# Optimization experiments

Hardware: AMD Instinct MI355X
Metric: run time of the kernel (lower is better)

The kernel has to match this reference:

```python
import jax, jax.numpy as jnp
import numpy as np

N, B, D = 50000, 128, 35   # nodes, graphs, node_dim
T = 140                     # padded sequence length
EPS = 1e-5

def _gcn(x, W, b, src, dst):
    # PyG GCNConv: sym-normalized adjacency with self loops, then linear.
    h = x @ W
    deg = jnp.ones((N,), h.dtype).at[dst].add(1.0)  # in-degree + self loop
    dinv = jax.lax.rsqrt(deg)
    msg = h[src] * (dinv[src] * dinv[dst])[:, None]
    agg = jax.ops.segment_sum(msg, dst, num_segments=N)
    return agg + h * (dinv * dinv)[:, None] + b  # + self-loop messages + bias

def _bn(x, g, b):
    m = x.mean(0)
    v = x.var(0)
    return (x - m) * jax.lax.rsqrt(v + EPS) * g + b

def _lstm(xs, Wih, Whh, bih, bhh, reverse):
    # xs: [T, B, D]; torch LSTM gate order i,f,g,o; hidden size D
    def step(carry, xt):
        h, c = carry
        gates = xt @ Wih.T + h @ Whh.T + bih + bhh
        i, f, g, o = jnp.split(gates, 4, axis=-1)
        c = jax.nn.sigmoid(f) * c + jax.nn.sigmoid(i) * jnp.tanh(g)
        h = jax.nn.sigmoid(o) * jnp.tanh(c)
        return (h, c), h
    h0 = jnp.zeros((xs.shape[1], D), xs.dtype)
    _, hs = jax.lax.scan(step, (h0, h0), xs, reverse=reverse)
    return hs

def setup_inputs() -> dict:
    key = jax.random.key(0)
    ks = iter(jax.random.split(key, 64))
    def w(shape, s=0.05):
        return jax.random.normal(next(ks), shape, jnp.float32) * s
    inp = {
        'x': jax.random.normal(next(ks), (N, D), jnp.float32),
        'edge_intra': jax.random.randint(next(ks), (2, 300000), 0, N, jnp.int32),
        'edge_inter': jax.random.randint(next(ks), (2, 100000), 0, N, jnp.int32),
        'split': jax.random.randint(next(ks), (N,), 0, 2, jnp.int32),
        'batch': jnp.sort(jax.random.randint(next(ks), (N,), 0, B, jnp.int32)),
    }
    dims = [(35, 128), (128, 256), (256, 512), (512, 256), (256, 35)]
    for i, (di, do) in enumerate(dims, 1):
        inp[f'W{i}'] = w((di, do)); inp[f'b{i}'] = jnp.zeros((do,), jnp.float32)
        inp[f'g{i}'] = jnp.ones((do,), jnp.float32); inp[f'be{i}'] = jnp.zeros((do,), jnp.float32)
    for d in ('f', 'b'):  # bidirectional LSTM, 4*D = 140 gate rows
        inp[f'Wih_{d}'] = w((4 * D, D)); inp[f'Whh_{d}'] = w((4 * D, D))
        inp[f'bih_{d}'] = jnp.zeros((4 * D,), jnp.float32); inp[f'bhh_{d}'] = jnp.zeros((4 * D,), jnp.float32)
    for nm in ('q', 'k', 'v'):  # attention over d=2*D=70
        inp[f'W{nm}'] = w((2 * D, 2 * D)); inp[f'b{nm}'] = jnp.zeros((2 * D,), jnp.float32)
    inp['Wfc1'] = w((9800, 4340), 0.01); inp['bfc1'] = jnp.zeros((4340,), jnp.float32)
    inp['Wfc2'] = w((4340, 1), 0.01); inp['bfc2'] = jnp.zeros((1,), jnp.float32)
    return inp

def reference(x, edge_intra, edge_inter, split, batch,
              W1, b1, g1, be1, W2, b2, g2, be2, W3, b3, g3, be3,
              W4, b4, g4, be4, W5, b5, g5, be5,
              Wih_f, Whh_f, bih_f, bhh_f, Wih_b, Whh_b, bih_b, bhh_b,
              Wq, bq, Wk, bk, Wv, bv, Wfc1, bfc1, Wfc2, bfc2):
    src = jnp.concatenate([edge_intra[0], edge_inter[0]])
    dst = jnp.concatenate([edge_intra[1], edge_inter[1]])
    # conv1-3: relu then bn; conv4: bn then relu; conv5: bn only
    h = _bn(jax.nn.relu(_gcn(x, W1, b1, src, dst)), g1, be1)
    h = _bn(jax.nn.relu(_gcn(h, W2, b2, src, dst)), g2, be2)
    h = _bn(jax.nn.relu(_gcn(h, W3, b3, src, dst)), g3, be3)
    h = jax.nn.relu(_bn(_gcn(h, W4, b4, src, dst), g4, be4))
    h = _bn(_gcn(h, W5, b5, src, dst), g5, be5)
    # masked global_add_pool per split (avoids dynamic boolean indexing)
    is_pro = (split == 1).astype(h.dtype)[:, None]
    pro = jax.ops.segment_sum(h * is_pro, batch, num_segments=B)
    lig = jax.ops.segment_sum(h * (1.0 - is_pro), batch, num_segments=B)
    seq = jnp.concatenate([lig, pro], axis=1).reshape(B, 2, D)  # L = 2
    seq = jnp.pad(seq, ((0, 0), (0, T - 2), (0, 0)))            # [B,140,35]
    # attention mask, L=2 (static)
    m = jnp.eye(T, dtype=jnp.float32)
    m = m.at[2:, :].set(0.0).at[:, 2:].set(0.0)
    m = m.at[:, 1].set(1.0).at[1, :].set(1.0).at[1, 1].set(0.0)
    # BiLSTM over time axis
    xs = seq.transpose(1, 0, 2)  # [T,B,35]
    hf = _lstm(xs, Wih_f, Whh_f, bih_f, bhh_f, False)
    hb = _lstm(xs, Wih_b, Whh_b, bih_b, bhh_b, True)
    out = jnp.concatenate([hf, hb], axis=-1).transpose(1, 0, 2)  # [B,140,70]
    # masked single-head attention
    q = out @ Wq + bq
    k = out @ Wk + bk
    v = out @ Wv + bv
    sc = jnp.einsum('bqd,bkd->bqk', q, k) / jnp.sqrt(jnp.asarray(2.0 * D, out.dtype))
    sc = jnp.where(m[None] == 0, -1e9, sc)
    o = jax.nn.softmax(sc, axis=-1) @ v  # [B,140,70]
    f = jax.nn.relu(o.reshape(B, -1) @ Wfc1 + bfc1)
    return (f @ Wfc2 + bfc2).reshape(-1)
```

## Files before the change

kernel.cpp:

```cpp
#include <hip/hip_runtime.h>

#define N_NODES 50000
#define DIM0 35
#define BGRAPH 128
#define TSEQ 140
#define EPSBN 1e-5f
#define E_TOTAL 400000
#define E_INTRA 300000
#define E_INTER 100000
#define FC1_OUT 4340

typedef __attribute__((ext_vector_type(8))) short s8v;
typedef __attribute__((ext_vector_type(4))) short s4v;
typedef __attribute__((ext_vector_type(4))) float f32x4;

static __device__ __forceinline__ unsigned short bf16_rne(float x) {
    unsigned int u = __float_as_uint(x);
    unsigned int r = (u + 0x7FFFu + ((u >> 16) & 1u)) >> 16;
    return (unsigned short)r;
}
static __device__ __forceinline__ void bf16_split(float x, unsigned short& h, unsigned short& l) {
    h = bf16_rne(x);
    float hf = __uint_as_float(((unsigned int)h) << 16);
    l = bf16_rne(x - hf);
}

static __device__ __forceinline__ void edge_sd(int e, const int* intra, const int* inter, int& s, int& d) {
    if (e < E_INTRA) { s = intra[e]; d = intra[E_INTRA + e]; }
    else { int k = e - E_INTRA; s = inter[k]; d = inter[E_INTER + k]; }
}

__global__ void k_init(int* cnt, int* cursor, float* out, const float* bfc2, float* bnsumAll, float* bv4) {
    int i = blockIdx.x * 256 + threadIdx.x;
    if (i < N_NODES) { cnt[i] = 0; cursor[i] = 0; }
    if (i < BGRAPH) out[i] = bfc2[0];
    if (i < 5 * 1024) bnsumAll[i] = 0.f;
    if (i < 256) bv4[i] = 0.f;
}

__global__ void k_deg(const int* intra, const int* inter, int* cnt) {
    int e = blockIdx.x * 256 + threadIdx.x;
    if (e >= E_TOTAL) return;
    int s, d; edge_sd(e, intra, inter, s, d);
    atomicAdd(&cnt[d], 1);
}

__global__ void k_scan1(const int* __restrict__ cnt, int* __restrict__ partial, int* __restrict__ blocksum,
                        float* __restrict__ dinv) {
    __shared__ int buf[256];
    int t = threadIdx.x;
    int i = blockIdx.x * 256 + t;
    int v = (i < N_NODES) ? cnt[i] : 0;
    if (i < N_NODES) dinv[i] = rsqrtf(1.0f + (float)v);
    buf[t] = v;
    __syncthreads();
    for (int off = 1; off < 256; off <<= 1) {
        int add = (t >= off) ? buf[t - off] : 0;
        __syncthreads();
        buf[t] += add;
        __syncthreads();
    }
    if (i < N_NODES) partial[i] = buf[t];
    if (t == 255) blocksum[blockIdx.x] = buf[255];
}

__global__ void k_scan2(int* blocksum, int nb) {
    __shared__ int buf[256];
    int t = threadIdx.x;
    buf[t] = (t < nb) ? blocksum[t] : 0;
    __syncthreads();
    for (int off = 1; off < 256; off <<= 1) {
        int add = (t >= off) ? buf[t - off] : 0;
        __syncthreads();
        buf[t] += add;
        __syncthreads();
    }
    if (t < nb) blocksum[t] = buf[t];
}

__global__ void k_scan3(const int* __restrict__ partial, const int* __restrict__ blocksum, int* __restrict__ rowptr) {
    int b = blockIdx.x;
    int i = b * 256 + threadIdx.x;
    if (i == 0) rowptr[0] = 0;
    if (i < N_NODES) {
        int off = (b == 0) ? 0 : blocksum[b - 1];
        rowptr[i + 1] = partial[i] + off;
    }
}

__global__ void k_scatter(const int* intra, const int* inter, const int* rowptr,
                          int* cursor, const float* dinv, int* srcs, float* coef) {
    int e = blockIdx.x * 256 + threadIdx.x;
    if (e >= E_TOTAL) return;
    int s, d; edge_sd(e, intra, inter, s, d);
    int p = rowptr[d] + atomicAdd(&cursor[d], 1);
    srcs[p] = s;
    coef[p] = dinv[s] * dinv[d];
}

__global__ __launch_bounds__(256) void k_agg_small(const float* __restrict__ X, float* __restrict__ Z,
        const int* __restrict__ rowptr, const int* __restrict__ srcs, const float* __restrict__ coef,
        const float* __restrict__ dinv, const float* __restrict__ bias) {
    int wave = threadIdx.x >> 6, lane = threadIdx.x & 63;
    int i = blockIdx.x * 4 + wave;
    if (i >= N_NODES || lane >= DIM0) return;
    int b0 = rowptr[i], e1 = rowptr[i + 1];
    float self = dinv[i] * dinv[i];
    float acc = X[(size_t)i * DIM0 + lane] * self;
    if (bias) acc += bias[lane];
    for (int k = b0; k < e1; ++k) acc += coef[k] * X[(size_t)srcs[k] * DIM0 + lane];
    Z[(size_t)i * DIM0 + lane] = acc;
}

__global__ __launch_bounds__(256) void k_agg_vec(const float* __restrict__ X, float* __restrict__ Z,
        const int* __restrict__ rowptr, const int* __restrict__ srcs, const float* __restrict__ coef,
        const float* __restrict__ dinv, const float* __restrict__ alpha, const float* __restrict__ beta,
        const float* __restrict__ bias, int d, int lpshift) {
    int i = (blockIdx.x * 256 + threadIdx.x) >> lpshift;
    int lane_in = threadIdx.x & ((1 << lpshift) - 1);
    if (i >= N_NODES) return;
    int b0 = rowptr[i], e1 = rowptr[i + 1];
    float self = dinv[i] * dinv[i];
    int c = lane_in * 4;
    float4 al, be;
    if (alpha) { al = *(const float4*)&alpha[c]; be = *(const float4*)&beta[c]; }
    else { al = make_float4(1.f, 1.f, 1.f, 1.f); be = make_float4(0.f, 0.f, 0.f, 0.f); }
    float4 xi = *(const float4*)&X[(size_t)i * d + c];
    float4 acc;
    acc.x = self * (al.x * xi.x + be.x);
    acc.y = self * (al.y * xi.y + be.y);
    acc.z = self * (al.z * xi.z + be.z);
    acc.w = self * (al.w * xi.w + be.w);
    if (bias) {
        float4 bi = *(const float4*)&bias[c];
        acc.x += bi.x; acc.y += bi.y; acc.z += bi.z; acc.w += bi.w;
    }
    for (int k = b0; k < e1; ++k) {
        int s = srcs[k];
        float cf = coef[k];
        float4 xs = *(const float4*)&X[(size_t)s * d + c];
        acc.x += cf * (al.x * xs.x + be.x);
        acc.y += cf * (al.y * xs.y + be.y);
        acc.z += cf * (al.z * xs.z + be.z);
        acc.w += cf * (al.w * xs.w + be.w);
    }
    *(float4*)&Z[(size_t)i * d + c] = acc;
}

__global__ __launch_bounds__(256) void k_gemm(const float* __restrict__ A, const float* __restrict__ W,
                                              const float* __restrict__ bias, float* __restrict__ C,
                                              int Mrows, int K, int Ncols, int relu,
                                              const float* __restrict__ alphaA, const float* __restrict__ betaA,
                                              int reluA) {
    __shared__ float As[64][17];
    __shared__ float Ws[16][65];
    int tid = threadIdx.x;
    int tx = tid & 15, ty = tid >> 4;
    int row0 = blockIdx.y * 64, col0 = blockIdx.x * 64;
    float acc[4][4] = {};
    for (int k0 = 0; k0 < K; k0 += 16) {
        for (int l = tid; l < 1024; l += 256) {
            int m = l >> 4, kk = l & 15;
            int r = row0 + m, k = k0 + kk;
            float v = 0.f;
            if (r < Mrows && k < K) {
                v = A[(size_t)r * K + k];
                if (alphaA) {
                    v = alphaA[k] * v + betaA[k];
                    if (reluA) v = fmaxf(v, 0.f);
                }
            }
            As[m][kk] = v;
        }
        for (int l = tid; l < 1024; l += 256) {
            int kk = l >> 6, n = l & 63;
            int k = k0 + kk, c = col0 + n;
            Ws[kk][n] = (k < K && c < Ncols) ? W[(size_t)k * Ncols + c] : 0.f;
        }
        __syncthreads();
#pragma unroll
        for (int kk = 0; kk < 16; ++kk) {
            float a[4], w[4];
#pragma unroll
            for (int i2 = 0; i2 < 4; ++i2) a[i2] = As[ty * 4 + i2][kk];
#pragma unroll
            for (int j = 0; j < 4; ++j) w[j] = Ws[kk][tx * 4 + j];
#pragma unroll
            for (int i2 = 0; i2 < 4; ++i2)
#pragma unroll
                for (int j = 0; j < 4; ++j)
                    acc[i2][j] += a[i2] * w[j];
        }
        __syncthreads();
    }
    for (int i2 = 0; i2 < 4; ++i2) {
        int r = row0 + ty * 4 + i2;
        if (r >= Mrows) continue;
        for (int j = 0; j < 4; ++j) {
            int c = col0 + tx * 4 + j;
            if (c >= Ncols) continue;
            float v = acc[i2][j];
            if (bias) v += bias[c];
            if (relu) v = fmaxf(v, 0.f);
            C[(size_t)r * Ncols + c] = v;
        }
    }
}

__global__ void k_wprep(const float* __restrict__ W, unsigned short* __restrict__ Wf, int K, int Ncols,
                        const float* __restrict__ rowscale) {
    int gid = blockIdx.x * 256 + threadIdx.x;
    int KT = K >> 5;
    int total = (Ncols >> 4) * KT * 64;
    if (gid >= total) return;
    int lane = gid & 63;
    int f = gid >> 6;
    int kt = f % KT, ntile = f / KT;
    int n = ntile * 16 + (lane & 15);
    int kb = kt * 32 + (lane >> 4) * 8;
    size_t base = (size_t)f * 1024 + lane * 8;
#pragma unroll
    for (int j = 0; j < 8; ++j) {
        float v = W[(size_t)(kb + j) * Ncols + n];
        if (rowscale) v *= rowscale[kb + j];
        unsigned short h, l;
        bf16_split(v, h, l);
        Wf[base + j] = h;
        Wf[base + 512 + j] = l;
    }
}

__global__ void k_bnbias(const float* __restrict__ W, const float* __restrict__ beta,
                         float* __restrict__ bv, int K, int Ncols) {
    int c = threadIdx.x;
    if (c >= Ncols) return;
    int k0 = blockIdx.x * 16;
    float acc = 0.f;
#pragma unroll
    for (int k = 0; k < 16; ++k) acc += beta[k0 + k] * W[(size_t)(k0 + k) * Ncols + c];
    atomicAdd(&bv[c], acc);
}

__global__ __launch_bounds__(256) void k_gemm_mfma(
    const float* __restrict__ A, const unsigned short* __restrict__ Wf,
    const float* __restrict__ bias, float* __restrict__ C,
    int Mrows, int K, int Ncols, int relu,
    const float* __restrict__ alphaA, const float* __restrict__ betaA,
    float* __restrict__ bnsum) {
    __shared__ unsigned short As[2][2][128][40];
    int tid = threadIdx.x;
    int lane = tid & 63, wave = tid >> 6;
    int wm = wave >> 1, wn = wave & 1;
    int row0 = blockIdx.y * 128;
    int nt0 = blockIdx.x * 8;
    int KT = K >> 5;

    f32x4 acc[4][4];
#pragma unroll
    for (int a = 0; a < 4; ++a)
#pragma unroll
        for (int b = 0; b < 4; ++b) acc[a][b] = (f32x4)0.f;

    float4 reg[4];
    auto load_chunk = [&](int kt) {
#pragma unroll
        for (int l = 0; l < 4; ++l) {
            int i = tid + l * 256;
            int m = i >> 3, kv = (i & 7) * 4;
            int r = row0 + m;
            float4 v = make_float4(0.f, 0.f, 0.f, 0.f);
            if (r < Mrows) v = *(const float4*)&A[(size_t)r * K + kt * 32 + kv];
            reg[l] = v;
        }
    };
    auto store_chunk = [&](int buf, int kt) {
#pragma unroll
        for (int l = 0; l < 4; ++l) {
            int i = tid + l * 256;
            int m = i >> 3, kv = (i & 7) * 4;
            float4 v = reg[l];
            if (alphaA) {
                int kg = kt * 32 + kv;
                float4 al = *(const float4*)&alphaA[kg];
                float4 be = *(const float4*)&betaA[kg];
                v.x = al.x * v.x + be.x;
                v.y = al.y * v.y + be.y;
                v.z = al.z * v.z + be.z;
                v.w = al.w * v.w + be.w;
            }
            unsigned short h0, l0, h1, l1, h2, l2, h3, l3;
            bf16_split(v.x, h0, l0); bf16_split(v.y, h1, l1);
            bf16_split(v.z, h2, l2); bf16_split(v.w, h3, l3);
            s4v hv = {(short)h0, (short)h1, (short)h2, (short)h3};
            s4v lv = {(short)l0, (short)l1, (short)l2, (short)l3};
            *(s4v*)&As[buf][0][m][kv] = hv;
            *(s4v*)&As[buf][1][m][kv] = lv;
        }
    };
    auto loadW = [&](int kt, s8v (&bh)[4], s8v (&bl)[4]) {
#pragma unroll
        for (int nt = 0; nt < 4; ++nt) {
            int ntg = nt0 + wn * 4 + nt;
            size_t fb = ((size_t)(ntg * KT + kt)) * 1024 + lane * 8;
            bh[nt] = *(const s8v*)&Wf[fb];
            bl[nt] = *(const s8v*)&Wf[fb + 512];
        }
    };

    int mrow = wm * 64 + (lane & 15);
    int koff = (lane >> 4) * 8;

    s8v bhA[4], blA[4], bhB[4], blB[4];
    load_chunk(0);
    store_chunk(0, 0);
    loadW(0, bhA, blA);
    __syncthreads();

    auto phase = [&](int kt, int cur, s8v (&bh)[4], s8v (&bl)[4], s8v (&nbh)[4], s8v (&nbl)[4]) {
        if (kt + 1 < KT) {
            load_chunk(kt + 1);
            loadW(kt + 1, nbh, nbl);
        }
        s8v ah[4], alo[4];
#pragma unroll
        for (int mt = 0; mt < 4; ++mt) {
            ah[mt]  = *(const s8v*)&As[cur][0][mrow + mt * 16][koff];
            alo[mt] = *(const s8v*)&As[cur][1][mrow + mt * 16][koff];
        }
#pragma unroll
        for (int nt = 0; nt < 4; ++nt)
#pragma unroll
            for (int mt = 0; mt < 4; ++mt) {
                acc[mt][nt] = __builtin_amdgcn_mfma_f32_16x16x32_bf16(ah[mt], bh[nt], acc[mt][nt], 0, 0, 0);
                acc[mt][nt] = __builtin_amdgcn_mfma_f32_16x16x32_bf16(ah[mt], bl[nt], acc[mt][nt], 0, 0, 0);
                acc[mt][nt] = __builtin_amdgcn_mfma_f32_16x16x32_bf16(alo[mt], bh[nt], acc[mt][nt], 0, 0, 0);
            }
        if (kt + 1 < KT) store_chunk(cur ^ 1, kt + 1);
        __syncthreads();
    };

    for (int kt = 0; kt < KT; kt += 2) {
        phase(kt, 0, bhA, blA, bhB, blB);
        phase(kt + 1, 1, bhB, blB, bhA, blA);
    }

    int cbase = (nt0 + wn * 4) * 16 + (lane & 15);
    float bia[4];
#pragma unroll
    for (int nt = 0; nt < 4; ++nt) bia[nt] = bias ? bias[cbase + nt * 16] : 0.f;
    float s1[4] = {0.f, 0.f, 0.f, 0.f}, s2[4] = {0.f, 0.f, 0.f, 0.f};
#pragma unroll
    for (int mt = 0; mt < 4; ++mt) {
        int rbase = row0 + wm * 64 + mt * 16 + (lane >> 4) * 4;
#pragma unroll
        for (int r = 0; r < 4; ++r) {
            int rg = rbase + r;
            if (rg < Mrows) {
#pragma unroll
                for (int nt = 0; nt < 4; ++nt) {
                    float v = acc[mt][nt][r] + bia[nt];
                    if (relu) v = fmaxf(v, 0.f);
                    C[(size_t)rg * Ncols + cbase + nt * 16] = v;
                    s1[nt] += v; s2[nt] += v * v;
                }
            }
        }
    }
    if (bnsum) {
#pragma unroll
        for (int nt = 0; nt < 4; ++nt) {
            float a = s1[nt], b = s2[nt];
            a += __shfl_xor(a, 16, 64);
            a += __shfl_xor(a, 32, 64);
            b += __shfl_xor(b, 16, 64);
            b += __shfl_xor(b, 32, 64);
            if (lane < 16) {
                atomicAdd(&bnsum[cbase + nt * 16], a);
                atomicAdd(&bnsum[Ncols + cbase + nt * 16], b);
            }
        }
    }
}

__global__ void k_bn_stats(const float* __restrict__ X, float* sums, int d) {
    long long total = (long long)N_NODES * d;
    int G = gridDim.x * blockDim.x;
    int gid = blockIdx.x * blockDim.x + threadIdx.x;
    int c = gid % d;
    float s1 = 0.f, s2 = 0.f;
    for (long long i = gid; i < total; i += G) {
        float v = X[i];
        s1 += v; s2 += v * v;
    }
    atomicAdd(&sums[c], s1);
    atomicAdd(&sums[d + c], s2);
}

__global__ void k_bn_final(const float* sums, const float* g, const float* be,
                           float* alpha, float* beta, int d) {
    int c = threadIdx.x;
    if (c >= d) return;
    float mean = sums[c] / (float)N_NODES;
    float var = sums[d + c] / (float)N_NODES - mean * mean;
    float a = g[c] * rsqrtf(var + EPSBN);
    alpha[c] = a;
    beta[c] = be[c] - mean * a;
}

__global__ void k_pool(const float* __restrict__ h, const int* __restrict__ split,
                       const int* __restrict__ batch, float* lig, float* pro,
                       const float* __restrict__ alpha, const float* __restrict__ beta) {
    int b = blockIdx.x;
    __shared__ float sl[DIM0], sp[DIM0];
    __shared__ int s_start, s_end;
    if (threadIdx.x < DIM0) { sl[threadIdx.x] = 0.f; sp[threadIdx.x] = 0.f; }
    if (threadIdx.x == 0) {
        int lo = 0, hi = N_NODES;
        while (lo < hi) { int mid = (lo + hi) >> 1; if (batch[mid] < b) lo = mid + 1; else hi = mid; }
        s_start = lo;
        hi = N_NODES;
        while (lo < hi) { int mid = (lo + hi) >> 1; if (batch[mid] < b + 1) lo = mid + 1; else hi = mid; }
        s_end = lo;
    }
    __syncthreads();
    int start = s_start, end = s_end;
    for (int k = threadIdx.x; k < (end - start) * DIM0; k += blockDim.x) {
        int node = start + k / DIM0;
        int c = k % DIM0;
        float v = alpha[c] * h[(size_t)node * DIM0 + c] + beta[c];
        if (split[node] == 1) atomicAdd(&sp[c], v);
        else atomicAdd(&sl[c], v);
    }
    __syncthreads();
    if (threadIdx.x < DIM0) {
        lig[b * DIM0 + threadIdx.x] = sl[threadIdx.x];
        pro[b * DIM0 + threadIdx.x] = sp[threadIdx.x];
    }
}

__global__ __launch_bounds__(192) void k_lstm(
    const float* __restrict__ lig, const float* __restrict__ pro,
    const float* __restrict__ Wih_f, const float* __restrict__ Whh_f,
    const float* __restrict__ bih_f, const float* __restrict__ bhh_f,
    const float* __restrict__ Wih_b, const float* __restrict__ Whh_b,
    const float* __restrict__ bih_b, const float* __restrict__ bhh_b,
    float* __restrict__ outb) {
    int blk = blockIdx.x;
    int dir = blk >> 7;
    int b = blk & 127;
    const float* Wih = dir ? Wih_b : Wih_f;
    const float* Whh = dir ? Whh_b : Whh_f;
    const float* bih = dir ? bih_b : bih_f;
    const float* bhh = dir ? bhh_b : bhh_f;

    __shared__ float h_lds[DIM0];
    __shared__ float x_lds[2][DIM0];
    __shared__ float gate_lds[4 * DIM0];
    int t = threadIdx.x;
    float wih[DIM0], whh[DIM0], bsum = 0.f;
    if (t < 4 * DIM0) {
#pragma unroll
        for (int j = 0; j < DIM0; ++j) { wih[j] = Wih[t * DIM0 + j]; whh[j] = Whh[t * DIM0 + j]; }
        bsum = bih[t] + bhh[t];
    }
    if (t < DIM0) {
        x_lds[0][t] = lig[b * DIM0 + t];
        x_lds[1][t] = pro[b * DIM0 + t];
        h_lds[t] = 0.f;
    }
    float c_reg = 0.f;
    __syncthreads();
    for (int step = 0; step < TSEQ; ++step) {
        int tt = dir ? (TSEQ - 1 - step) : step;
        if (t < 4 * DIM0) {
            float acc = bsum;
            if (tt < 2) {
#pragma unroll
                for (int j = 0; j < DIM0; ++j) acc += wih[j] * x_lds[tt][j];
            }
#pragma unroll
            for (int j = 0; j < DIM0; ++j) acc += whh[j] * h_lds[j];
            gate_lds[t] = acc;
        }
        __syncthreads();
        if (t < DIM0) {
            float gi = gate_lds[t], gf = gate_lds[DIM0 + t];
            float gg = gate_lds[2 * DIM0 + t], go = gate_lds[3 * DIM0 + t];
            float si = 1.f / (1.f + expf(-gi));
            float sf = 1.f / (1.f + expf(-gf));
            float so = 1.f / (1.f + expf(-go));
            c_reg = sf * c_reg + si * tanhf(gg);
            float hv = so * tanhf(c_reg);
            h_lds[t] = hv;
            outb[((size_t)b * TSEQ + tt) * 70 + dir * DIM0 + t] = hv;
        }
        __syncthreads();
    }
}

__global__ void k_concatW(const float* __restrict__ Wq, const float* __restrict__ bq,
                          const float* __restrict__ Wk, const float* __restrict__ bk,
                          const float* __restrict__ Wv, const float* __restrict__ bv,
                          float* __restrict__ Wcat, float* __restrict__ bcat) {
    int idx = blockIdx.x * 256 + threadIdx.x;
    if (idx < 70 * 210) {
        int k = idx / 210, col = idx % 210;
        int g = col / 70, j = col % 70;
        const float* Wsrc = (g == 0) ? Wq : ((g == 1) ? Wk : Wv);
        Wcat[idx] = Wsrc[k * 70 + j];
    }
    if (idx < 210) {
        int g = idx / 70, j = idx % 70;
        const float* bsrc = (g == 0) ? bq : ((g == 1) ? bk : bv);
        bcat[idx] = bsrc[j];
    }
}

__global__ void k_attention(const float* __restrict__ qkv, float* __restrict__ osm) {
    int b = blockIdx.x;
    __shared__ float q0[70], q1[70], s[TSEQ];
    __shared__ float s00_s, s01_s, ssum_s;
    int t = threadIdx.x;
    const float* base = qkv + (size_t)b * TSEQ * 210;
    if (t < 70) {
        q0[t] = base[0 * 210 + t];
        q1[t] = base[1 * 210 + t];
    }
    __syncthreads();
    const float scale = rsqrtf(70.f);
    if (t < TSEQ) {
        const float* krow = base + (size_t)t * 210 + 70;
        float acc = 0.f;
        for (int j = 0; j < 70; ++j) acc += q1[j] * krow[j];
        s[t] = acc * scale;
    } else if (t == TSEQ || t == TSEQ + 1) {
        int kk = t - TSEQ;
        const float* krow = base + (size_t)kk * 210 + 70;
        float acc = 0.f;
        for (int j = 0; j < 70; ++j) acc += q0[j] * krow[j];
        if (kk) s01_s = acc * scale; else s00_s = acc * scale;
    }
    __syncthreads();
    if (t == 0) {
        float mx = -1e30f;
        for (int i = 0; i < TSEQ; ++i) if (i != 1) mx = fmaxf(mx, s[i]);
        float sum = 0.f;
        for (int i = 0; i < TSEQ; ++i) {
            float e = (i == 1) ? 0.f : expf(s[i] - mx);
            s[i] = e; sum += e;
        }
        ssum_s = sum;
    }
    __syncthreads();
    if (t < 70) {
        float inv = 1.f / ssum_s;
        float acc = 0.f;
        for (int i = 0; i < TSEQ; ++i) acc += s[i] * base[(size_t)i * 210 + 140 + t];
        float o1v = acc * inv;
        float m0 = fmaxf(s00_s, s01_s);
        float e0 = expf(s00_s - m0), e1 = expf(s01_s - m0);
        float w0 = e0 / (e0 + e1), w1 = e1 / (e0 + e1);
        float v0 = base[0 * 210 + 140 + t];
        float v1 = base[1 * 210 + 140 + t];
        osm[b * 210 + t] = w0 * v0 + w1 * v1;
        osm[b * 210 + 70 + t] = o1v;
        osm[b * 210 + 140 + t] = v1;
    }
}

__global__ void k_wsum(const float* __restrict__ Wfc1, float* __restrict__ Wsum) {
    int idx = blockIdx.x * 256 + threadIdx.x;
    if (idx >= 70 * FC1_OUT) return;
    int j = idx / FC1_OUT, c = idx % FC1_OUT;
    float acc = 0.f;
    for (int tt = 2; tt < TSEQ; ++tt) acc += Wfc1[((size_t)(tt * 70 + j)) * FC1_OUT + c];
    Wsum[(size_t)j * FC1_OUT + c] = acc;
}

__global__ __launch_bounds__(256) void k_fc(const float* __restrict__ osm, const float* __restrict__ Wfc1,
                                            const float* __restrict__ Wsum, const float* __restrict__ bfc1,
                                            const float* __restrict__ Wfc2, float* __restrict__ out) {
    __shared__ float olds[8][210];
    __shared__ float wred[4][8];
    int g = blockIdx.y;
    int c = blockIdx.x * 256 + threadIdx.x;
    for (int l = threadIdx.x; l < 8 * 210; l += 256)
        olds[l / 210][l % 210] = osm[(g * 8 + l / 210) * 210 + (l % 210)];
    __syncthreads();
    float acc[8] = {};
    if (c < FC1_OUT) {
        for (int j = 0; j < 140; ++j) {
            float w = Wfc1[(size_t)j * FC1_OUT + c];
#pragma unroll
            for (int b = 0; b < 8; ++b) acc[b] = fmaf(olds[b][j], w, acc[b]);
        }
        for (int j = 0; j < 70; ++j) {
            float w = Wsum[(size_t)j * FC1_OUT + c];
#pragma unroll
            for (int b = 0; b < 8; ++b) acc[b] = fmaf(olds[b][140 + j], w, acc[b]);
        }
        float bb = bfc1[c], pw = Wfc2[c];
#pragma unroll
        for (int b = 0; b < 8; ++b) acc[b] = fmaxf(acc[b] + bb, 0.f) * pw;
    }
#pragma unroll
    for (int b = 0; b < 8; ++b) {
        acc[b] += __shfl_down(acc[b], 32, 64);
        acc[b] += __shfl_down(acc[b], 16, 64);
        acc[b] += __shfl_down(acc[b], 8, 64);
        acc[b] += __shfl_down(acc[b], 4, 64);
        acc[b] += __shfl_down(acc[b], 2, 64);
        acc[b] += __shfl_down(acc[b], 1, 64);
    }
    int wave = threadIdx.x >> 6;
    if ((threadIdx.x & 63) == 0)
#pragma unroll
        for (int b = 0; b < 8; ++b) wred[wave][b] = acc[b];
    __syncthreads();
    if (threadIdx.x < 8) {
        float t = wred[0][threadIdx.x] + wred[1][threadIdx.x] + wred[2][threadIdx.x] + wred[3][threadIdx.x];
        atomicAdd(&out[g * 8 + threadIdx.x], t);
    }
}

extern "C" void kernel_launch(void* const* d_in, const int* in_sizes, int n_in,
                              void* d_out, int out_size, void* d_ws, size_t ws_size,
                              hipStream_t stream) {
    const float* x = (const float*)d_in[0];
    const int* intra = (const int*)d_in[1];
    const int* inter = (const int*)d_in[2];
    const int* split = (const int*)d_in[3];
    const int* batch = (const int*)d_in[4];
    const float *W[5], *bW[5], *gW[5], *beW[5];
    for (int i = 0; i < 5; ++i) {
        W[i]   = (const float*)d_in[5 + 4 * i];
        bW[i]  = (const float*)d_in[6 + 4 * i];
        gW[i]  = (const float*)d_in[7 + 4 * i];
        beW[i] = (const float*)d_in[8 + 4 * i];
    }
    const float* Wih_f = (const float*)d_in[25];
    const float* Whh_f = (const float*)d_in[26];
    const float* bih_f = (const float*)d_in[27];
    const float* bhh_f = (const float*)d_in[28];
    const float* Wih_b = (const float*)d_in[29];
    const float* Whh_b = (const float*)d_in[30];
    const float* bih_b = (const float*)d_in[31];
    const float* bhh_b = (const float*)d_in[32];
    const float* Wq = (const float*)d_in[33];
    const float* bq = (const float*)d_in[34];
    const float* Wk = (const float*)d_in[35];
    const float* bk = (const float*)d_in[36];
    const float* Wv = (const float*)d_in[37];
    const float* bv = (const float*)d_in[38];
    const float* Wfc1 = (const float*)d_in[39];
    const float* bfc1 = (const float*)d_in[40];
    const float* Wfc2 = (const float*)d_in[41];
    const float* bfc2 = (const float*)d_in[42];

    char* p = (char*)d_ws;
    auto carve = [&](size_t bytes) {
        char* r = p;
        p += (bytes + 255) & ~(size_t)255;
        return r;
    };
    float* bufA = (float*)carve((size_t)N_NODES * 512 * 4);
    float* bufB = (float*)carve((size_t)N_NODES * 256 * 4);
    float* bufM = (float*)carve((size_t)N_NODES * 256 * 4);
    float* dinv = (float*)carve((size_t)N_NODES * 4);
    int* cnt    = (int*)carve((size_t)N_NODES * 4);
    int* rowptr = (int*)carve((size_t)(N_NODES + 1) * 4);
    int* cursor = (int*)carve((size_t)N_NODES * 4);
    int* scanp  = (int*)carve((size_t)N_NODES * 4);
    int* bsums  = (int*)carve(256 * 4);
    int* srcs   = (int*)carve((size_t)E_TOTAL * 4);
    float* coef = (float*)carve((size_t)E_TOTAL * 4);
    float* bnsumAll = (float*)carve(5 * 1024 * 4);
    float* alphaAll = (float*)carve(5 * 512 * 4);
    float* betaAll  = (float*)carve(5 * 512 * 4);
    float* bv4  = (float*)carve(256 * 4);
    float* lig = (float*)carve((size_t)BGRAPH * DIM0 * 4);
    float* pro = (float*)carve((size_t)BGRAPH * DIM0 * 4);
    float* outb = (float*)carve((size_t)BGRAPH * TSEQ * 70 * 4);
    float* qkvb = (float*)carve((size_t)BGRAPH * TSEQ * 210 * 4);
    float* Wcat = (float*)carve((size_t)70 * 210 * 4);
    float* bcat = (float*)carve(210 * 4);
    float* osm = (float*)carve((size_t)BGRAPH * 210 * 4);
    float* wsum = (float*)carve((size_t)70 * FC1_OUT * 4);
    unsigned short* Wf2 = (unsigned short*)carve((size_t)128 * 256 * 2 * 2);
    unsigned short* Wf3 = (unsigned short*)carve((size_t)256 * 512 * 2 * 2);
    unsigned short* Wf4 = (unsigned short*)carve((size_t)512 * 256 * 2 * 2);

    float* out = (float*)d_out;

    const int SCAN_B = (N_NODES + 255) / 256;

    k_init<<<(N_NODES + 255) / 256, 256, 0, stream>>>(cnt, cursor, out, bfc2, bnsumAll, bv4);
    k_deg<<<(E_TOTAL + 255) / 256, 256, 0, stream>>>(intra, inter, cnt);
    k_scan1<<<SCAN_B, 256, 0, stream>>>(cnt, scanp, bsums, dinv);
    k_scan2<<<1, 256, 0, stream>>>(bsums, SCAN_B);
    k_scan3<<<SCAN_B, 256, 0, stream>>>(scanp, bsums, rowptr);
    k_scatter<<<(E_TOTAL + 255) / 256, 256, 0, stream>>>(intra, inter, rowptr, cursor, dinv, srcs, coef);
    k_concatW<<<(70 * 210 + 255) / 256, 256, 0, stream>>>(Wq, bq, Wk, bk, Wv, bv, Wcat, bcat);
    k_wprep<<<((256 / 16) * (128 / 32) * 64 + 255) / 256, 256, 0, stream>>>(W[1], Wf2, 128, 256, nullptr);
    k_wprep<<<((512 / 16) * (256 / 32) * 64 + 255) / 256, 256, 0, stream>>>(W[2], Wf3, 256, 512, nullptr);

    auto BN = [&](int layer) { return bnsumAll + layer * 1024; };
    auto AL = [&](int layer) { return alphaAll + layer * 512; };
    auto BE = [&](int layer) { return betaAll + layer * 512; };
    auto bn_final = [&](int layer, int d) {
        k_bn_final<<<1, 512, 0, stream>>>(BN(layer), gW[layer], beW[layer], AL(layer), BE(layer), d);
    };

    const int GB64 = (N_NODES + 63) / 64;
    const int GB128 = (N_NODES + 127) / 128;
    const int AGG4 = (N_NODES + 3) / 4;
    const int AGG8 = (N_NODES + 7) / 8;

    k_agg_small<<<AGG4, 256, 0, stream>>>(x, bufM, rowptr, srcs, coef, dinv, nullptr);
    k_gemm<<<dim3(2, GB64), 256, 0, stream>>>(bufM, W[0], bW[0], bufA, N_NODES, 35, 128, 1, nullptr, nullptr, 0);
    k_bn_stats<<<128, 256, 0, stream>>>(bufA, BN(0), 128);
    bn_final(0, 128);
    k_agg_vec<<<AGG8, 256, 0, stream>>>(bufA, bufM, rowptr, srcs, coef, dinv, AL(0), BE(0), nullptr, 128, 5);
    k_gemm_mfma<<<dim3(2, GB128), 256, 0, stream>>>(bufM, Wf2, bW[1], bufB, N_NODES, 128, 256, 1,
                                                    nullptr, nullptr, BN(1));
    bn_final(1, 256);
    k_agg_vec<<<AGG4, 256, 0, stream>>>(bufB, bufM, rowptr, srcs, coef, dinv, AL(1), BE(1), nullptr, 256, 6);
    k_gemm_mfma<<<dim3(4, GB128), 256, 0, stream>>>(bufM, Wf3, bW[2], bufA, N_NODES, 256, 512, 1,
                                                    nullptr, nullptr, BN(2));
    bn_final(2, 512);
    k_wprep<<<((256 / 16) * (512 / 32) * 64 + 255) / 256, 256, 0, stream>>>(W[3], Wf4, 512, 256, AL(2));
    k_bnbias<<<512 / 16, 256, 0, stream>>>(W[3], BE(2), bv4, 512, 256);
    k_gemm_mfma<<<dim3(2, GB128), 256, 0, stream>>>(bufA, Wf4, bv4, bufM, N_NODES, 512, 256, 0,
                                                    nullptr, nullptr, nullptr);
    k_agg_vec<<<AGG4, 256, 0, stream>>>(bufM, bufB, rowptr, srcs, coef, dinv, nullptr, nullptr, bW[3], 256, 6);
    k_bn_stats<<<256, 256, 0, stream>>>(bufB, BN(3), 256);
    bn_final(3, 256);
    k_gemm<<<dim3(1, GB64), 256, 0, stream>>>(bufB, W[4], nullptr, bufM, N_NODES, 256, 35, 0, AL(3), BE(3), 1);
    k_agg_small<<<AGG4, 256, 0, stream>>>(bufM, bufA, rowptr, srcs, coef, dinv, bW[4]);
    k_bn_stats<<<35, 256, 0, stream>>>(bufA, BN(4), 35);
    bn_final(4, 35);

    k_pool<<<BGRAPH, 256, 0, stream>>>(bufA, split, batch, lig, pro, AL(4), BE(4));

    k_lstm<<<256, 192, 0, stream>>>(lig, pro, Wih_f, Whh_f, bih_f, bhh_f,
                                    Wih_b, Whh_b, bih_b, bhh_b, outb);

    k_gemm<<<dim3(4, (BGRAPH * TSEQ + 63) / 64), 256, 0, stream>>>(outb, Wcat, bcat, qkvb,
                                                                   BGRAPH * TSEQ, 70, 210, 0, nullptr, nullptr, 0);

    k_attention<<<BGRAPH, 256, 0, stream>>>(qkvb, osm);

    k_wsum<<<(70 * FC1_OUT + 255) / 256, 256, 0, stream>>>(Wfc1, wsum);
    k_fc<<<dim3(17, 16), 256, 0, stream>>>(osm, Wfc1, wsum, bfc1, Wfc2, out);
}
```

Measured before the change: 1.017 ms.

## Fuse BN finalize into consumers, fold BN stats into GEMM, misc tweaks

Removes the separate k_bn_final launches and recomputes the BN scale/shift inline from the raw sums wherever they are consumed (aggregation, GEMM loaders, weight prep, pool). The first layer's k_bn_stats pass is folded into the scalar GEMM epilogue through shared-memory and global atomics. Edge-loop bounds in the aggregation kernels are made wave-uniform with readfirstlane, and the LSTM recurrent dot product is split across two accumulators to shorten the dependency chain. The cost is redundant per-element rsqrt work in hot loaders and extra atomics in the GEMM epilogue.

```diff
diff --git a/kernel.cpp b/kernel.cpp
--- a/kernel.cpp
+++ b/kernel.cpp
@@ -24,6 +24,14 @@
     float hf = __uint_as_float(((unsigned int)h) << 16);
     l = bf16_rne(x - hf);
 }
+static __device__ __forceinline__ void bn_ab(const float* __restrict__ bnsum, const float* __restrict__ g,
+                                             const float* __restrict__ be, int d, int c, float& a, float& b) {
+    const float invN = 1.0f / (float)N_NODES;
+    float mean = bnsum[c] * invN;
+    float var = bnsum[d + c] * invN - mean * mean;
+    a = g[c] * rsqrtf(var + EPSBN);
+    b = be[c] - mean * a;
+}
 
 static __device__ __forceinline__ void edge_sd(int e, const int* intra, const int* inter, int& s, int& d) {
     if (e < E_INTRA) { s = intra[e]; d = intra[E_INTRA + e]; }
@@ -104,7 +112,8 @@
     int wave = threadIdx.x >> 6, lane = threadIdx.x & 63;
     int i = blockIdx.x * 4 + wave;
     if (i >= N_NODES || lane >= DIM0) return;
-    int b0 = rowptr[i], e1 = rowptr[i + 1];
+    int b0 = __builtin_amdgcn_readfirstlane(rowptr[i]);
+    int e1 = __builtin_amdgcn_readfirstlane(rowptr[i + 1]);
     float self = dinv[i] * dinv[i];
     float acc = X[(size_t)i * DIM0 + lane] * self;
     if (bias) acc += bias[lane];
@@ -114,23 +123,32 @@
 
 __global__ __launch_bounds__(256) void k_agg_vec(const float* __restrict__ X, float* __restrict__ Z,
         const int* __restrict__ rowptr, const int* __restrict__ srcs, const float* __restrict__ coef,
-        const float* __restrict__ dinv, const float* __restrict__ alpha, const float* __restrict__ beta,
-        const float* __restrict__ bias, int d, int lpshift) {
+        const float* __restrict__ dinv, const float* __restrict__ bnsum, const float* __restrict__ g,
+        const float* __restrict__ be, const float* __restrict__ bias, int d, int lpshift) {
     int i = (blockIdx.x * 256 + threadIdx.x) >> lpshift;
     int lane_in = threadIdx.x & ((1 << lpshift) - 1);
     if (i >= N_NODES) return;
     int b0 = rowptr[i], e1 = rowptr[i + 1];
+    if (lpshift == 6) {
+        b0 = __builtin_amdgcn_readfirstlane(b0);
+        e1 = __builtin_amdgcn_readfirstlane(e1);
+    }
     float self = dinv[i] * dinv[i];
     int c = lane_in * 4;
-    float4 al, be;
-    if (alpha) { al = *(const float4*)&alpha[c]; be = *(const float4*)&beta[c]; }
-    else { al = make_float4(1.f, 1.f, 1.f, 1.f); be = make_float4(0.f, 0.f, 0.f, 0.f); }
+    float4 al = make_float4(1.f, 1.f, 1.f, 1.f);
+    float4 bb = make_float4(0.f, 0.f, 0.f, 0.f);
+    if (bnsum) {
+        bn_ab(bnsum, g, be, d, c + 0, al.x, bb.x);
+        bn_ab(bnsum, g, be, d, c + 1, al.y, bb.y);
+        bn_ab(bnsum, g, be, d, c + 2, al.z, bb.z);
+        bn_ab(bnsum, g, be, d, c + 3, al.w, bb.w);
+    }
     float4 xi = *(const float4*)&X[(size_t)i * d + c];
     float4 acc;
-    acc.x = self * (al.x * xi.x + be.x);
-    acc.y = self * (al.y * xi.y + be.y);
-    acc.z = self * (al.z * xi.z + be.z);
-    acc.w = self * (al.w * xi.w + be.w);
+    acc.x = self * (al.x * xi.x + bb.x);
+    acc.y = self * (al.y * xi.y + bb.y);
+    acc.z = self * (al.z * xi.z + bb.z);
+    acc.w = self * (al.w * xi.w + bb.w);
     if (bias) {
         float4 bi = *(const float4*)&bias[c];
         acc.x += bi.x; acc.y += bi.y; acc.z += bi.z; acc.w += bi.w;
@@ -139,10 +157,10 @@
         int s = srcs[k];
         float cf = coef[k];
         float4 xs = *(const float4*)&X[(size_t)s * d + c];
-        acc.x += cf * (al.x * xs.x + be.x);
-        acc.y += cf * (al.y * xs.y + be.y);
-        acc.z += cf * (al.z * xs.z + be.z);
-        acc.w += cf * (al.w * xs.w + be.w);
+        acc.x += cf * (al.x * xs.x + bb.x);
+        acc.y += cf * (al.y * xs.y + bb.y);
+        acc.z += cf * (al.z * xs.z + bb.z);
+        acc.w += cf * (al.w * xs.w + bb.w);
     }
     *(float4*)&Z[(size_t)i * d + c] = acc;
 }
@@ -150,13 +168,16 @@
 __global__ __launch_bounds__(256) void k_gemm(const float* __restrict__ A, const float* __restrict__ W,
                                               const float* __restrict__ bias, float* __restrict__ C,
                                               int Mrows, int K, int Ncols, int relu,
-                                              const float* __restrict__ alphaA, const float* __restrict__ betaA,
-                                              int reluA) {
+                                              const float* __restrict__ bnA, const float* __restrict__ gA,
+                                              const float* __restrict__ beA, int reluA,
+                                              float* __restrict__ bnsumOut) {
     __shared__ float As[64][17];
     __shared__ float Ws[16][65];
+    __shared__ float sl_s[64], sq_s[64];
     int tid = threadIdx.x;
     int tx = tid & 15, ty = tid >> 4;
     int row0 = blockIdx.y * 64, col0 = blockIdx.x * 64;
+    if (tid < 64) { sl_s[tid] = 0.f; sq_s[tid] = 0.f; }
     float acc[4][4] = {};
     for (int k0 = 0; k0 < K; k0 += 16) {
         for (int l = tid; l < 1024; l += 256) {
@@ -165,8 +186,10 @@
             float v = 0.f;
             if (r < Mrows && k < K) {
                 v = A[(size_t)r * K + k];
-                if (alphaA) {
-                    v = alphaA[k] * v + betaA[k];
+                if (bnA) {
+                    float a, b;
+                    bn_ab(bnA, gA, beA, K, k, a, b);
+                    v = a * v + b;
                     if (reluA) v = fmaxf(v, 0.f);
                 }
             }
@@ -193,6 +216,7 @@
         }
         __syncthreads();
     }
+    float s1l[4] = {0.f, 0.f, 0.f, 0.f}, s2l[4] = {0.f, 0.f, 0.f, 0.f};
     for (int i2 = 0; i2 < 4; ++i2) {
         int r = row0 + ty * 4 + i2;
         if (r >= Mrows) continue;
@@ -203,12 +227,28 @@
             if (bias) v += bias[c];
             if (relu) v = fmaxf(v, 0.f);
             C[(size_t)r * Ncols + c] = v;
+            s1l[j] += v; s2l[j] += v * v;
+        }
+    }
+    if (bnsumOut) {
+#pragma unroll
+        for (int j = 0; j < 4; ++j) {
+            atomicAdd(&sl_s[tx * 4 + j], s1l[j]);
+            atomicAdd(&sq_s[tx * 4 + j], s2l[j]);
+        }
+        __syncthreads();
+        if (tid < 64) {
+            int c = col0 + tid;
+            if (c < Ncols) {
+                atomicAdd(&bnsumOut[c], sl_s[tid]);
+                atomicAdd(&bnsumOut[Ncols + c], sq_s[tid]);
+            }
         }
     }
 }
 
 __global__ void k_wprep(const float* __restrict__ W, unsigned short* __restrict__ Wf, int K, int Ncols,
-                        const float* __restrict__ rowscale) {
+                        const float* __restrict__ bnR, const float* __restrict__ gR, const float* __restrict__ beR) {
     int gid = blockIdx.x * 256 + threadIdx.x;
     int KT = K >> 5;
     int total = (Ncols >> 4) * KT * 64;
@@ -222,7 +262,11 @@
 #pragma unroll
     for (int j = 0; j < 8; ++j) {
         float v = W[(size_t)(kb + j) * Ncols + n];
-        if (rowscale) v *= rowscale[kb + j];
+        if (bnR) {
+            float a, b;
+            bn_ab(bnR, gR, beR, K, kb + j, a, b);
+            v *= a;
+        }
         unsigned short h, l;
         bf16_split(v, h, l);
         Wf[base + j] = h;
@@ -230,14 +274,19 @@
     }
 }
 
-__global__ void k_bnbias(const float* __restrict__ W, const float* __restrict__ beta,
+__global__ void k_bnbias(const float* __restrict__ W, const float* __restrict__ bnR,
+                         const float* __restrict__ gR, const float* __restrict__ beR,
                          float* __restrict__ bv, int K, int Ncols) {
     int c = threadIdx.x;
     if (c >= Ncols) return;
     int k0 = blockIdx.x * 16;
     float acc = 0.f;
 #pragma unroll
-    for (int k = 0; k < 16; ++k) acc += beta[k0 + k] * W[(size_t)(k0 + k) * Ncols + c];
+    for (int k = 0; k < 16; ++k) {
+        float a, b;
+        bn_ab(bnR, gR, beR, K, k0 + k, a, b);
+        acc += b * W[(size_t)(k0 + k) * Ncols + c];
+    }
     atomicAdd(&bv[c], acc);
 }
 
@@ -245,7 +294,7 @@
     const float* __restrict__ A, const unsigned short* __restrict__ Wf,
     const float* __restrict__ bias, float* __restrict__ C,
     int Mrows, int K, int Ncols, int relu,
-    const float* __restrict__ alphaA, const float* __restrict__ betaA,
+    const float* __restrict__ bnA, const float* __restrict__ gA, const float* __restrict__ beA,
     float* __restrict__ bnsum) {
     __shared__ unsigned short As[2][2][128][40];
     int tid = threadIdx.x;
@@ -279,14 +328,17 @@
             int i = tid + l * 256;
             int m = i >> 3, kv = (i & 7) * 4;
             float4 v = reg[l];
-            if (alphaA) {
+            if (bnA) {
                 int kg = kt * 32 + kv;
-                float4 al = *(const float4*)&alphaA[kg];
-                float4 be = *(const float4*)&betaA[kg];
-                v.x = al.x * v.x + be.x;
-                v.y = al.y * v.y + be.y;
-                v.z = al.z * v.z + be.z;
-                v.w = al.w * v.w + be.w;
+                float a0, b0n, a1, b1, a2, b2, a3, b3;
+                bn_ab(bnA, gA, beA, K, kg + 0, a0, b0n);
+                bn_ab(bnA, gA, beA, K, kg + 1, a1, b1);
+                bn_ab(bnA, gA, beA, K, kg + 2, a2, b2);
+                bn_ab(bnA, gA, beA, K, kg + 3, a3, b3);
+                v.x = a0 * v.x + b0n;
+                v.y = a1 * v.y + b1;
+                v.z = a2 * v.z + b2;
+                v.w = a3 * v.w + b3;
             }
             unsigned short h0, l0, h1, l1, h2, l2, h3, l3;
             bf16_split(v.x, h0, l0); bf16_split(v.y, h1, l1);
@@ -396,24 +448,19 @@
     atomicAdd(&sums[d + c], s2);
 }
 
-__global__ void k_bn_final(const float* sums, const float* g, const float* be,
-                           float* alpha, float* beta, int d) {
-    int c = threadIdx.x;
-    if (c >= d) return;
-    float mean = sums[c] / (float)N_NODES;
-    float var = sums[d + c] / (float)N_NODES - mean * mean;
-    float a = g[c] * rsqrtf(var + EPSBN);
-    alpha[c] = a;
-    beta[c] = be[c] - mean * a;
-}
-
 __global__ void k_pool(const float* __restrict__ h, const int* __restrict__ split,
                        const int* __restrict__ batch, float* lig, float* pro,
-                       const float* __restrict__ alpha, const float* __restrict__ beta) {
+                       const float* __restrict__ bnsum, const float* __restrict__ g,
+                       const float* __restrict__ be) {
     int b = blockIdx.x;
-    __shared__ float sl[DIM0], sp[DIM0];
+    __shared__ float sl[DIM0], sp[DIM0], aL[DIM0], bL[DIM0];
     __shared__ int s_start, s_end;
-    if (threadIdx.x < DIM0) { sl[threadIdx.x] = 0.f; sp[threadIdx.x] = 0.f; }
+    if (threadIdx.x < DIM0) {
+        sl[threadIdx.x] = 0.f; sp[threadIdx.x] = 0.f;
+        float a, bb;
+        bn_ab(bnsum, g, be, DIM0, threadIdx.x, a, bb);
+        aL[threadIdx.x] = a; bL[threadIdx.x] = bb;
+    }
     if (threadIdx.x == 0) {
         int lo = 0, hi = N_NODES;
         while (lo < hi) { int mid = (lo + hi) >> 1; if (batch[mid] < b) lo = mid + 1; else hi = mid; }
@@ -427,7 +474,7 @@
     for (int k = threadIdx.x; k < (end - start) * DIM0; k += blockDim.x) {
         int node = start + k / DIM0;
         int c = k % DIM0;
-        float v = alpha[c] * h[(size_t)node * DIM0 + c] + beta[c];
+        float v = aL[c] * h[(size_t)node * DIM0 + c] + bL[c];
         if (split[node] == 1) atomicAdd(&sp[c], v);
         else atomicAdd(&sl[c], v);
     }
@@ -473,14 +520,18 @@
     for (int step = 0; step < TSEQ; ++step) {
         int tt = dir ? (TSEQ - 1 - step) : step;
         if (t < 4 * DIM0) {
-            float acc = bsum;
+            float acc0 = bsum, acc1 = 0.f;
             if (tt < 2) {
 #pragma unroll
-                for (int j = 0; j < DIM0; ++j) acc += wih[j] * x_lds[tt][j];
+                for (int j = 0; j < DIM0; ++j) acc0 += wih[j] * x_lds[tt][j];
             }
 #pragma unroll
-            for (int j = 0; j < DIM0; ++j) acc += whh[j] * h_lds[j];
-            gate_lds[t] = acc;
+            for (int j = 0; j < DIM0 - 1; j += 2) {
+                acc0 += whh[j] * h_lds[j];
+                acc1 += whh[j + 1] * h_lds[j + 1];
+            }
+            acc0 += whh[DIM0 - 1] * h_lds[DIM0 - 1];
+            gate_lds[t] = acc0 + acc1;
         }
         __syncthreads();
         if (t < DIM0) {
@@ -675,8 +726,6 @@
     int* srcs   = (int*)carve((size_t)E_TOTAL * 4);
     float* coef = (float*)carve((size_t)E_TOTAL * 4);
     float* bnsumAll = (float*)carve(5 * 1024 * 4);
-    float* alphaAll = (float*)carve(5 * 512 * 4);
-    float* betaAll  = (float*)carve(5 * 512 * 4);
     float* bv4  = (float*)carve(256 * 4);
     float* lig = (float*)carve((size_t)BGRAPH * DIM0 * 4);
     float* pro = (float*)carve((size_t)BGRAPH * DIM0 * 4);
@@ -701,15 +750,12 @@
     k_scan3<<<SCAN_B, 256, 0, stream>>>(scanp, bsums, rowptr);
     k_scatter<<<(E_TOTAL + 255) / 256, 256, 0, stream>>>(intra, inter, rowptr, cursor, dinv, srcs, coef);
     k_concatW<<<(70 * 210 + 255) / 256, 256, 0, stream>>>(Wq, bq, Wk, bk, Wv, bv, Wcat, bcat);
-    k_wprep<<<((256 / 16) * (128 / 32) * 64 + 255) / 256, 256, 0, stream>>>(W[1], Wf2, 128, 256, nullptr);
-    k_wprep<<<((512 / 16) * (256 / 32) * 64 + 255) / 256, 256, 0, stream>>>(W[2], Wf3, 256, 512, nullptr);
+    k_wprep<<<((256 / 16) * (128 / 32) * 64 + 255) / 256, 256, 0, stream>>>(W[1], Wf2, 128, 256,
+                                                                            nullptr, nullptr, nullptr);
+    k_wprep<<<((512 / 16) * (256 / 32) * 64 + 255) / 256, 256, 0, stream>>>(W[2], Wf3, 256, 512,
+                                                                            nullptr, nullptr, nullptr);
 
     auto BN = [&](int layer) { return bnsumAll + layer * 1024; };
-    auto AL = [&](int layer) { return alphaAll + layer * 512; };
-    auto BE = [&](int layer) { return betaAll + layer * 512; };
-    auto bn_final = [&](int layer, int d) {
-        k_bn_final<<<1, 512, 0, stream>>>(BN(layer), gW[layer], beW[layer], AL(layer), BE(layer), d);
-    };
 
     const int GB64 = (N_NODES + 63) / 64;
     const int GB128 = (N_NODES + 127) / 128;
@@ -717,36 +763,37 @@
     const int AGG8 = (N_NODES + 7) / 8;
 
     k_agg_small<<<AGG4, 256, 0, stream>>>(x, bufM, rowptr, srcs, coef, dinv, nullptr);
-    k_gemm<<<dim3(2, GB64), 256, 0, stream>>>(bufM, W[0], bW[0], bufA, N_NODES, 35, 128, 1, nullptr, nullptr, 0);
-    k_bn_stats<<<128, 256, 0, stream>>>(bufA, BN(0), 128);
-    bn_final(0, 128);
-    k_agg_vec<<<AGG8, 256, 0, stream>>>(bufA, bufM, rowptr, srcs, coef, dinv, AL(0), BE(0), nullptr, 128, 5);
+    k_gemm<<<dim3(2, GB64), 256, 0, stream>>>(bufM, W[0], bW[0], bufA, N_NODES, 35, 128, 1,
+                                              nullptr, nullptr, nullptr, 0, BN(0));
+    k_agg_vec<<<AGG8, 256, 0, stream>>>(bufA, bufM, rowptr, srcs, coef, dinv, BN(0), gW[0], beW[0],
+                                        nullptr, 128, 5);
     k_gemm_mfma<<<dim3(2, GB128), 256, 0, stream>>>(bufM, Wf2, bW[1], bufB, N_NODES, 128, 256, 1,
-                                                    nullptr, nullptr, BN(1));
-    bn_final(1, 256);
-    k_agg_vec<<<AGG4, 256, 0, stream>>>(bufB, bufM, rowptr, srcs, coef, dinv, AL(1), BE(1), nullptr, 256, 6);
+                                                    nullptr, nullptr, nullptr, BN(1));
+    k_agg_vec<<<AGG4, 256, 0, stream>>>(bufB, bufM, rowptr, srcs, coef, dinv, BN(1), gW[1], beW[1],
+                                        nullptr, 256, 6);
     k_gemm_mfma<<<dim3(4, GB128), 256, 0, stream>>>(bufM, Wf3, bW[2], bufA, N_NODES, 256, 512, 1,
-                                                    nullptr, nullptr, BN(2));
-    bn_final(2, 512);
-    k_wprep<<<((256 / 16) * (512 / 32) * 64 + 255) / 256, 256, 0, stream>>>(W[3], Wf4, 512, 256, AL(2));
-    k_bnbias<<<512 / 16, 256, 0, stream>>>(W[3], BE(2), bv4, 512, 256);
+                                                    nullptr, nullptr, nullptr, BN(2));
+    k_wprep<<<((256 / 16) * (512 / 32) * 64 + 255) / 256, 256, 0, stream>>>(W[3], Wf4, 512, 256,
+                                                                            BN(2), gW[2], beW[2]);
+    k_bnbias<<<512 / 16, 256, 0, stream>>>(W[3], BN(2), gW[2], beW[2], bv4, 512, 256);
     k_gemm_mfma<<<dim3(2, GB128), 256, 0, stream>>>(bufA, Wf4, bv4, bufM, N_NODES, 512, 256, 0,
-                                                    nullptr, nullptr, nullptr);
-    k_agg_vec<<<AGG4, 256, 0, stream>>>(bufM, bufB, rowptr, srcs, coef, dinv, nullptr, nullptr, bW[3], 256, 6);
+                                                    nullptr, nullptr, nullptr, nullptr);
+    k_agg_vec<<<AGG4, 256, 0, stream>>>(bufM, bufB, rowptr, srcs, coef, dinv, nullptr, nullptr, nullptr,
+                                        bW[3], 256, 6);
     k_bn_stats<<<256, 256, 0, stream>>>(bufB, BN(3), 256);
-    bn_final(3, 256);
-    k_gemm<<<dim3(1, GB64), 256, 0, stream>>>(bufB, W[4], nullptr, bufM, N_NODES, 256, 35, 0, AL(3), BE(3), 1);
+    k_gemm<<<dim3(1, GB64), 256, 0, stream>>>(bufB, W[4], nullptr, bufM, N_NODES, 256, 35, 0,
+                                              BN(3), gW[3], beW[3], 1, nullptr);
     k_agg_small<<<AGG4, 256, 0, stream>>>(bufM, bufA, rowptr, srcs, coef, dinv, bW[4]);
     k_bn_stats<<<35, 256, 0, stream>>>(bufA, BN(4), 35);
-    bn_final(4, 35);
-
-    k_pool<<<BGRAPH, 256, 0, stream>>>(bufA, split, batch, lig, pro, AL(4), BE(4));
+
+    k_pool<<<BGRAPH, 256, 0, stream>>>(bufA, split, batch, lig, pro, BN(4), gW[4], beW[4]);
 
     k_lstm<<<256, 192, 0, stream>>>(lig, pro, Wih_f, Whh_f, bih_f, bhh_f,
                                     Wih_b, Whh_b, bih_b, bhh_b, outb);
 
     k_gemm<<<dim3(4, (BGRAPH * TSEQ + 63) / 64), 256, 0, stream>>>(outb, Wcat, bcat, qkvb,
-                                                                   BGRAPH * TSEQ, 70, 210, 0, nullptr, nullptr, 0);
+                                                                   BGRAPH * TSEQ, 70, 210, 0,
+                                                                   nullptr, nullptr, nullptr, 0, nullptr);
 
     k_attention<<<BGRAPH, 256, 0, stream>>>(qkvb, osm);
 
```

After: 1.183 ms. 16.3% more time.
